# Kernel optimization log

Hardware: AMD Instinct MI355X
Metric: run time of the kernel (lower is better)

Reference implementation:

```python
import jax, jax.numpy as jnp
from jax import lax
import numpy as np

EPS = 0.01      # entropic regularization (points live in [0,1]^3, sq-dists <= 3)
N_ITERS = 50    # fixed Sinkhorn iterations (approximate matching)


def setup_inputs() -> dict:
    key = jax.random.key(0)
    kx, ky = jax.random.split(key)
    x = jax.random.uniform(kx, (16, 2048, 3), dtype=jnp.float32)
    y = jax.random.uniform(ky, (16, 2048, 3), dtype=jnp.float32)
    return {"x": x, "y": y}


def _emd(x, y):
    # x, y: [B, N, 3] point clouds. Approximate EMD via entropic OT (log-domain Sinkhorn).
    # Pairwise squared Euclidean cost: [B, N, N]
    C = jnp.sum((x[:, :, None, :] - y[:, None, :, :]) ** 2, axis=-1)
    B, N, _ = C.shape
    log_marg = -jnp.log(jnp.asarray(N, C.dtype))  # uniform marginals 1/N

    f0 = jnp.zeros((B, N), C.dtype)
    g0 = jnp.zeros((B, N), C.dtype)

    def step(carry, _):
        f, g = carry
        # f_i = eps * (log a_i - logsumexp_j (g_j - C_ij)/eps)
        f = EPS * (log_marg - jax.nn.logsumexp((g[:, None, :] - C) / EPS, axis=2))
        # g_j = eps * (log b_j - logsumexp_i (f_i - C_ij)/eps)
        g = EPS * (log_marg - jax.nn.logsumexp((f[:, :, None] - C) / EPS, axis=1))
        return (f, g), None

    (f, g), _ = lax.scan(step, (f0, g0), None, length=N_ITERS)

    # Transport plan P_ij = exp((f_i + g_j - C_ij)/eps); EMD = <P, C> per batch
    P = jnp.exp((f[:, :, None] + g[:, None, :] - C) / EPS)
    return jnp.sum(P * C, axis=(1, 2))  # [B]


def reference(x, y):
    return _emd(x, y)
```

## Files before the change

### kernel.cpp

```cpp
#include <hip/hip_runtime.h>

#define NPTS 2048
#define NB   16
#define WGS  1024
#define ARRV 16

typedef float v2f __attribute__((ext_vector_type(2)));

constexpr float K_R       = 144.26950408889634f;
constexpr float K_TWO_R   = 288.53900817779268f;
constexpr float K_INV2R   = 0.0034657359027997264f;
constexpr float K_EPS_LN2 = 0.0069314718055994531f;

__device__ __forceinline__ float fexp2(float x) { return __builtin_amdgcn_exp2f(x); }
__device__ __forceinline__ float flog2(float x) { return __builtin_amdgcn_logf(x); }

__device__ __forceinline__ float aload(const float* p) {
    return __hip_atomic_load(p, __ATOMIC_RELAXED, __HIP_MEMORY_SCOPE_AGENT);
}
__device__ __forceinline__ v2f aload2(const float* p) {
    unsigned long long v = __hip_atomic_load((const unsigned long long*)p,
                           __ATOMIC_RELAXED, __HIP_MEMORY_SCOPE_AGENT);
    union { unsigned long long u; v2f f; } c; c.u = v; return c.f;
}
__device__ __forceinline__ void astore(float* p, float v) {
    __hip_atomic_store(p, v, __ATOMIC_RELAXED, __HIP_MEMORY_SCOPE_AGENT);
}

__global__ __launch_bounds__(256) void prep_kernel(
    const float* __restrict__ x, const float* __restrict__ y,
    float4* __restrict__ px, float4* __restrict__ py, float* __restrict__ g)
{
    int idx = blockIdx.x * 256 + threadIdx.x;
    if (idx >= NB * NPTS) return;
    float x0 = x[idx*3+0], x1 = x[idx*3+1], x2 = x[idx*3+2];
    float xx = fmaf(x0,x0, fmaf(x1,x1, x2*x2));
    px[idx] = make_float4(x0*K_TWO_R, x1*K_TWO_R, x2*K_TWO_R, -xx*K_R);
    float y0 = y[idx*3+0], y1 = y[idx*3+1], y2 = y[idx*3+2];
    float yy = fmaf(y0,y0, fmaf(y1,y1, y2*y2));
    py[idx] = make_float4(y0*K_TWO_R, y1*K_TWO_R, y2*K_TWO_R, -yy*K_R);
    g[idx] = -yy*K_R;
}

__device__ __forceinline__ void batch_barrier(unsigned* ctr, unsigned target) {
    __syncthreads();
    if (threadIdx.x == 0) {
        asm volatile("s_waitcnt vmcnt(0)" ::: "memory");
        __hip_atomic_fetch_add(ctr, 1u, __ATOMIC_RELAXED, __HIP_MEMORY_SCOPE_AGENT);
        while (__hip_atomic_load(ctr, __ATOMIC_RELAXED, __HIP_MEMORY_SCOPE_AGENT)
               < target)
            __builtin_amdgcn_s_sleep(1);
        asm volatile("" ::: "memory");
    }
    __syncthreads();
}

__global__ __launch_bounds__(1024) void sinkhorn_fused(
    const float4* __restrict__ px4, const float4* __restrict__ py4,
    float* __restrict__ f, float* __restrict__ g,
    unsigned* __restrict__ bar, float* __restrict__ out)
{
    __shared__ v2f vyx[1024], vyy[1024], vyz[1024], vyw[1024];
    __shared__ v2f vxx[1024], vxy[1024], vxz[1024];
    __shared__ v2f vhw[1024];
    __shared__ v2f rowp[1024];
    __shared__ float wsum[16];

    const int bid   = blockIdx.x;
    const int b     = bid >> 4;
    const int chunk = bid & 15;
    const int tid   = threadIdx.x;
    const int lane  = tid & 63;
    const int wid   = tid >> 6;
    const int row0  = chunk * 128 + wid * 8;

    const float4* pyb = py4 + b * NPTS;
    const float4* pxb = px4 + b * NPTS;
    float* fb = f + b * NPTS;
    float* gb = g + b * NPTS;
    unsigned* ctr = bar + b * 64;

    #pragma unroll
    for (int i2 = 0; i2 < 2; ++i2) {
        int k = i2 * WGS + tid;
        float4 p = pyb[k];
        ((float*)vyx)[k] = p.x; ((float*)vyy)[k] = p.y;
        ((float*)vyz)[k] = p.z; ((float*)vyw)[k] = p.w;
        float4 q2 = pxb[k];
        ((float*)vxx)[k] = q2.x; ((float*)vxy)[k] = q2.y;
        ((float*)vxz)[k] = q2.z;
    }
    {
        int ph  = tid >> 9;
        int w16 = (tid >> 5) & 15;
        int r   = (tid >> 2) & 7;
        int cp  = tid & 3;
        float4 p = (ph ? pyb : pxb)[chunk * 128 + w16 * 8 + r];
        float v = (cp == 0) ? p.x * K_INV2R :
                  (cp == 1) ? p.y * K_INV2R :
                  (cp == 2) ? p.z * K_INV2R : p.w;
        v2f t; t.x = v; t.y = v;
        rowp[(ph * 16 + w16) * 32 + r * 4 + cp] = t;
    }

    auto run_phase = [&](const v2f* PX, const v2f* PY, const v2f* PZ,
                         int ph, float* dual_out) {
        v2f rx2[8], ry2[8], rz2[8], u02[8];
        const v2f* rp = &rowp[(ph * 16 + wid) * 32];
        #pragma unroll
        for (int r = 0; r < 8; ++r) {
            rx2[r] = rp[r*4+0]; ry2[r] = rp[r*4+1];
            rz2[r] = rp[r*4+2]; u02[r] = rp[r*4+3];
        }
        v2f acc2[8];
        #pragma unroll
        for (int r = 0; r < 8; ++r) { acc2[r].x = 0.f; acc2[r].y = 0.f; }

        #pragma unroll 2
        for (int c = 0; c < 16; ++c) {
            int jp = c * 64 + lane;
            v2f X = PX[jp], Y = PY[jp], Z = PZ[jp], H = vhw[jp];
            #pragma unroll
            for (int r = 0; r < 8; ++r) {
                v2f w = Z * rz2[r] + (H + u02[r]);
                w = Y * ry2[r] + w;
                w = X * rx2[r] + w;
                v2f e; e.x = fexp2(w.x); e.y = fexp2(w.y);
                acc2[r] += e;
            }
        }

        float sv[8];
        #pragma unroll
        for (int r = 0; r < 8; ++r) {
            float s = acc2[r].x + acc2[r].y;
            #pragma unroll
            for (int off = 1; off < 64; off <<= 1)
                s += __shfl_xor(s, off, 64);
            sv[r] = s;
        }
        if (lane < 8) {
            float s = sv[0];
            #pragma unroll
            for (int r = 1; r < 8; ++r) s = (lane == r) ? sv[r] : s;
            float u0s = ((const float*)&rp[lane * 4 + 3])[0];
            astore(&dual_out[lane], -11.0f - flog2(s) + u0s);
        }
    };

    unsigned tgt = ARRV;
    for (int it = 0; it < 50; ++it) {
        vhw[tid] = aload2(&gb[2 * tid]);
        __syncthreads();
        run_phase(vyx, vyy, vyz, 0, &fb[row0]);
        batch_barrier(ctr, tgt); tgt += ARRV;

        vhw[tid] = aload2(&fb[2 * tid]);
        __syncthreads();
        run_phase(vxx, vxy, vxz, 1, &gb[row0]);
        batch_barrier(ctr, tgt); tgt += ARRV;
    }

    vhw[tid] = aload2(&gb[2 * tid]);
    const v2f* rpf = &rowp[wid * 32];
    float fR[8];
    #pragma unroll
    for (int r = 0; r < 8; ++r) {
        float xw = ((const float*)&rpf[r * 4 + 3])[0];
        fR[r] = aload(&fb[row0 + r]) - xw;
    }
    __syncthreads();

    {
        v2f rx2[8], ry2[8], rz2[8], u02[8];
        #pragma unroll
        for (int r = 0; r < 8; ++r) {
            rx2[r] = rpf[r*4+0]; ry2[r] = rpf[r*4+1];
            rz2[r] = rpf[r*4+2]; u02[r] = rpf[r*4+3];
        }
        v2f accE; accE.x = 0.f; accE.y = 0.f;
        #pragma unroll 2
        for (int c = 0; c < 16; ++c) {
            int jp = c * 64 + lane;
            v2f X = vyx[jp], Y = vyy[jp], Z = vyz[jp];
            v2f H = vhw[jp], YW = vyw[jp];
            #pragma unroll
            for (int r = 0; r < 8; ++r) {
                v2f w = Z * rz2[r] + (H + u02[r]);
                w = Y * ry2[r] + w;
                w = X * rx2[r] + w;
                v2f cr = (H - YW) - w;
                v2f e;
                e.x = fexp2(w.x + fR[r]) * cr.x;
                e.y = fexp2(w.y + fR[r]) * cr.y;
                accE += e;
            }
        }
        float s = accE.x + accE.y;
        #pragma unroll
        for (int off = 1; off < 64; off <<= 1) s += __shfl_xor(s, off, 64);
        if (lane == 0) wsum[wid] = s;
        __syncthreads();
        if (tid == 0) {
            float t = 0.f;
            #pragma unroll
            for (int i2 = 0; i2 < 16; ++i2) t += wsum[i2];
            atomicAdd(&out[b], t * K_EPS_LN2);
        }
    }
}

extern "C" void kernel_launch(void* const* d_in, const int* in_sizes, int n_in,
                              void* d_out, int out_size, void* d_ws, size_t ws_size,
                              hipStream_t stream)
{
    const float* x = (const float*)d_in[0];
    const float* y = (const float*)d_in[1];
    float* out = (float*)d_out;

    char* ws = (char*)d_ws;
    float4*   px  = (float4*)(ws);
    float4*   py  = (float4*)(ws + (size_t)NB * NPTS * 16);
    float*    f   = (float*)  (ws + (size_t)NB * NPTS * 32);
    float*    g   = (float*)  (ws + (size_t)NB * NPTS * 32 + (size_t)NB * NPTS * 4);
    unsigned* bar = (unsigned*)(ws + (size_t)NB * NPTS * 32 + (size_t)NB * NPTS * 8);

    hipMemsetAsync(d_out, 0, (size_t)out_size * sizeof(float), stream);
    hipMemsetAsync(bar, 0, NB * 64 * sizeof(unsigned), stream);

    prep_kernel<<<(NB * NPTS + 255) / 256, 256, 0, stream>>>(x, y, px, py, g);
    sinkhorn_fused<<<NB * ARRV, WGS, 0, stream>>>(px, py, f, g, bar, out);
}
```

Measured before the change: 1.166 ms.

## Replace per-batch global barrier with per-wave dataflow flags for Sinkhorn phases

The workgroup-wide global barrier between Sinkhorn half-steps is replaced by per-wave counters in global memory. Each wave waits only for the 16 producer waves whose dual values it loads, and publishes its slice through workgroup-scope LDS flags, so the other waves can start on the slices that are ready while the rest are still arriving. Parity double-buffering of the dual array in LDS lets consecutive phases overlap. This removes the __syncthreads and barrier stalls, at the cost of more spin-polling traffic, finer-grained memory-ordering reasoning, and 256 counters per batch.

```diff
diff --git a/kernel.cpp b/kernel.cpp
--- a/kernel.cpp
+++ b/kernel.cpp
@@ -3,7 +3,6 @@
 #define NPTS 2048
 #define NB   16
 #define WGS  1024
-#define ARRV 16
 
 typedef float v2f __attribute__((ext_vector_type(2)));
 
@@ -24,6 +23,12 @@
     union { unsigned long long u; v2f f; } c; c.u = v; return c.f;
 }
 __device__ __forceinline__ void astore(float* p, float v) {
+    __hip_atomic_store(p, v, __ATOMIC_RELAXED, __HIP_MEMORY_SCOPE_AGENT);
+}
+__device__ __forceinline__ unsigned aloadu(const unsigned* p) {
+    return __hip_atomic_load(p, __ATOMIC_RELAXED, __HIP_MEMORY_SCOPE_AGENT);
+}
+__device__ __forceinline__ void astoreu(unsigned* p, unsigned v) {
     __hip_atomic_store(p, v, __ATOMIC_RELAXED, __HIP_MEMORY_SCOPE_AGENT);
 }
 
@@ -42,19 +47,6 @@
     g[idx] = -yy*K_R;
 }
 
-__device__ __forceinline__ void batch_barrier(unsigned* ctr, unsigned target) {
-    __syncthreads();
-    if (threadIdx.x == 0) {
-        asm volatile("s_waitcnt vmcnt(0)" ::: "memory");
-        __hip_atomic_fetch_add(ctr, 1u, __ATOMIC_RELAXED, __HIP_MEMORY_SCOPE_AGENT);
-        while (__hip_atomic_load(ctr, __ATOMIC_RELAXED, __HIP_MEMORY_SCOPE_AGENT)
-               < target)
-            __builtin_amdgcn_s_sleep(1);
-        asm volatile("" ::: "memory");
-    }
-    __syncthreads();
-}
-
 __global__ __launch_bounds__(1024) void sinkhorn_fused(
     const float4* __restrict__ px4, const float4* __restrict__ py4,
     float* __restrict__ f, float* __restrict__ g,
@@ -62,23 +54,25 @@
 {
     __shared__ v2f vyx[1024], vyy[1024], vyz[1024], vyw[1024];
     __shared__ v2f vxx[1024], vxy[1024], vxz[1024];
-    __shared__ v2f vhw[1024];
+    __shared__ v2f vhw2[2048];
     __shared__ v2f rowp[1024];
+    __shared__ unsigned fl[16];
     __shared__ float wsum[16];
 
-    const int bid   = blockIdx.x;
-    const int b     = bid >> 4;
-    const int chunk = bid & 15;
-    const int tid   = threadIdx.x;
-    const int lane  = tid & 63;
-    const int wid   = tid >> 6;
-    const int row0  = chunk * 128 + wid * 8;
+    const int bid  = blockIdx.x;
+    const int b    = bid >> 4;
+    const int q    = bid & 15;
+    const int tid  = threadIdx.x;
+    const int lane = tid & 63;
+    const int wid  = tid >> 6;
+    const int row0 = q * 128 + wid * 8;
 
     const float4* pyb = py4 + b * NPTS;
     const float4* pxb = px4 + b * NPTS;
     float* fb = f + b * NPTS;
     float* gb = g + b * NPTS;
-    unsigned* ctr = bar + b * 64;
+    unsigned* ctrb  = bar + b * 256;
+    unsigned* myctr = ctrb + q * 16 + wid;
 
     #pragma unroll
     for (int i2 = 0; i2 < 2; ++i2) {
@@ -95,18 +89,40 @@
         int w16 = (tid >> 5) & 15;
         int r   = (tid >> 2) & 7;
         int cp  = tid & 3;
-        float4 p = (ph ? pyb : pxb)[chunk * 128 + w16 * 8 + r];
+        float4 p = (ph ? pyb : pxb)[q * 128 + w16 * 8 + r];
         float v = (cp == 0) ? p.x * K_INV2R :
                   (cp == 1) ? p.y * K_INV2R :
                   (cp == 2) ? p.z * K_INV2R : p.w;
         v2f t; t.x = v; t.y = v;
         rowp[(ph * 16 + w16) * 32 + r * 4 + cp] = t;
     }
-
-    auto run_phase = [&](const v2f* PX, const v2f* PY, const v2f* PZ,
-                         int ph, float* dual_out) {
+    if (tid < 16) fl[tid] = 0;
+    __syncthreads();
+
+    for (int t = 0; t < 100; ++t) {
+        const int par = t & 1;
+        const float* din = par ? fb : gb;
+        float*      dout = par ? gb : fb;
+        const v2f* PX = par ? vxx : vyx;
+        const v2f* PY = par ? vxy : vyy;
+        const v2f* PZ = par ? vxz : vyz;
+        v2f* HB = &vhw2[par * 1024];
+        const v2f* rp = &rowp[(par * 16 + wid) * 32];
+
+        if (t > 0) {
+            const unsigned* cl = ctrb + wid * 16;
+            for (;;) {
+                unsigned v = (lane < 16) ? aloadu(&cl[lane]) : ~0u;
+                if (__all((int)(v >= (unsigned)t))) break;
+                __builtin_amdgcn_s_sleep(2);
+            }
+        }
+        HB[wid * 64 + lane] = aload2(&din[wid * 128 + 2 * lane]);
+        if (lane == 0)
+            __hip_atomic_store(&fl[wid], (unsigned)(t + 1),
+                               __ATOMIC_RELEASE, __HIP_MEMORY_SCOPE_WORKGROUP);
+
         v2f rx2[8], ry2[8], rz2[8], u02[8];
-        const v2f* rp = &rowp[(ph * 16 + wid) * 32];
         #pragma unroll
         for (int r = 0; r < 8; ++r) {
             rx2[r] = rp[r*4+0]; ry2[r] = rp[r*4+1];
@@ -116,10 +132,16 @@
         #pragma unroll
         for (int r = 0; r < 8; ++r) { acc2[r].x = 0.f; acc2[r].y = 0.f; }
 
-        #pragma unroll 2
-        for (int c = 0; c < 16; ++c) {
-            int jp = c * 64 + lane;
-            v2f X = PX[jp], Y = PY[jp], Z = PZ[jp], H = vhw[jp];
+        for (int s = 0; s < 16; ++s) {
+            int k = (wid + s) & 15;
+            if (s) {
+                while (__hip_atomic_load(&fl[k], __ATOMIC_ACQUIRE,
+                                         __HIP_MEMORY_SCOPE_WORKGROUP)
+                       < (unsigned)(t + 1))
+                    __builtin_amdgcn_s_sleep(1);
+            }
+            int jp = k * 64 + lane;
+            v2f X = PX[jp], Y = PY[jp], Z = PZ[jp], H = HB[jp];
             #pragma unroll
             for (int r = 0; r < 8; ++r) {
                 v2f w = Z * rz2[r] + (H + u02[r]);
@@ -144,24 +166,20 @@
             #pragma unroll
             for (int r = 1; r < 8; ++r) s = (lane == r) ? sv[r] : s;
             float u0s = ((const float*)&rp[lane * 4 + 3])[0];
-            astore(&dual_out[lane], -11.0f - flog2(s) + u0s);
-        }
-    };
-
-    unsigned tgt = ARRV;
-    for (int it = 0; it < 50; ++it) {
-        vhw[tid] = aload2(&gb[2 * tid]);
-        __syncthreads();
-        run_phase(vyx, vyy, vyz, 0, &fb[row0]);
-        batch_barrier(ctr, tgt); tgt += ARRV;
-
-        vhw[tid] = aload2(&fb[2 * tid]);
-        __syncthreads();
-        run_phase(vxx, vxy, vxz, 1, &gb[row0]);
-        batch_barrier(ctr, tgt); tgt += ARRV;
-    }
-
-    vhw[tid] = aload2(&gb[2 * tid]);
+            astore(&dout[row0 + lane], -11.0f - flog2(s) + u0s);
+        }
+        asm volatile("s_waitcnt vmcnt(0)" ::: "memory");
+        if (lane == 0) astoreu(myctr, (unsigned)(t + 1));
+    }
+
+    for (int k2 = 0; k2 < 16; ++k2) {
+        const unsigned* cl = ctrb + k2 * 16;
+        for (;;) {
+            unsigned v = (lane < 16) ? aloadu(&cl[lane]) : ~0u;
+            if (__all((int)(v >= 100u))) break;
+            __builtin_amdgcn_s_sleep(2);
+        }
+    }
     const v2f* rpf = &rowp[wid * 32];
     float fR[8];
     #pragma unroll
@@ -169,8 +187,6 @@
         float xw = ((const float*)&rpf[r * 4 + 3])[0];
         fR[r] = aload(&fb[row0 + r]) - xw;
     }
-    __syncthreads();
-
     {
         v2f rx2[8], ry2[8], rz2[8], u02[8];
         #pragma unroll
@@ -182,8 +198,8 @@
         #pragma unroll 2
         for (int c = 0; c < 16; ++c) {
             int jp = c * 64 + lane;
-            v2f X = vyx[jp], Y = vyy[jp], Z = vyz[jp];
-            v2f H = vhw[jp], YW = vyw[jp];
+            v2f H = aload2(&gb[2 * jp]);
+            v2f X = vyx[jp], Y = vyy[jp], Z = vyz[jp], YW = vyw[jp];
             #pragma unroll
             for (int r = 0; r < 8; ++r) {
                 v2f w = Z * rz2[r] + (H + u02[r]);
@@ -202,10 +218,10 @@
         if (lane == 0) wsum[wid] = s;
         __syncthreads();
         if (tid == 0) {
-            float t = 0.f;
-            #pragma unroll
-            for (int i2 = 0; i2 < 16; ++i2) t += wsum[i2];
-            atomicAdd(&out[b], t * K_EPS_LN2);
+            float t2 = 0.f;
+            #pragma unroll
+            for (int i2 = 0; i2 < 16; ++i2) t2 += wsum[i2];
+            atomicAdd(&out[b], t2 * K_EPS_LN2);
         }
     }
 }
@@ -226,8 +242,8 @@
     unsigned* bar = (unsigned*)(ws + (size_t)NB * NPTS * 32 + (size_t)NB * NPTS * 8);
 
     hipMemsetAsync(d_out, 0, (size_t)out_size * sizeof(float), stream);
-    hipMemsetAsync(bar, 0, NB * 64 * sizeof(unsigned), stream);
+    hipMemsetAsync(bar, 0, NB * 256 * sizeof(unsigned), stream);
 
     prep_kernel<<<(NB * NPTS + 255) / 256, 256, 0, stream>>>(x, y, px, py, g);
-    sinkhorn_fused<<<NB * ARRV, WGS, 0, stream>>>(px, py, f, g, bar, out);
-}
+    sinkhorn_fused<<<NB * 16, WGS, 0, stream>>>(px, py, f, g, bar, out);
+}
```

Measured after the change: 1.335 ms. +14.5%, slower.
